# Kernel tuning notes

Measured on AMD Instinct MI355X. Metric: run time of the kernel, lower is better.

Reference implementation:

```python
import jax, jax.numpy as jnp
import numpy as np

S = 15.0  # hard-coded scale in HELoss.__init__


def setup_inputs() -> dict:
    key = jax.random.key(0)
    k1, k2, k3 = jax.random.split(key, 3)
    B, C = 4096, 32000
    logits = jax.random.normal(k1, (B, C), dtype=jnp.float32)
    labels = jax.random.randint(k2, (B,), 0, C, dtype=jnp.int64)
    cm = jax.random.uniform(k3, (), dtype=jnp.float32)
    return {"logits": logits, "labels": labels, "cm": cm}


def reference(logits, labels, cm):
    # logits: [B, C], labels: [B] int, cm: scalar margin
    B, C = logits.shape
    # diagonal gather: logits[i, labels[i]]
    tgt = jnp.take_along_axis(logits, labels[:, None], axis=1)[:, 0]  # [B]
    numerator = S * (tgt - cm)  # [B]
    # masked exp-sum over non-target classes (replaces the per-row cat loop)
    col = jnp.arange(C)[None, :]
    is_tgt = labels[:, None] == col  # [B, C] bool
    ex = jnp.where(is_tgt, 0.0, jnp.exp(S * logits))
    denom = jnp.exp(numerator) + jnp.sum(ex, axis=1)  # [B]
    return -jnp.mean(numerator - jnp.log(denom))
```

## Files before the change

### kernel.cpp

```cpp
#include <hip/hip_runtime.h>
#include <math.h>

#define SCALE_S 15.0f

__device__ __forceinline__ void combine_ms(float& m, float& s, float m2, float s2) {
    float nm = fmaxf(m, m2);
    s = s * __expf(m - nm) + s2 * __expf(m2 - nm);
    m = nm;
}

__global__ __launch_bounds__(256) void heloss_row_kernel(
        const float* __restrict__ logits,
        const int* __restrict__ labels,
        const float* __restrict__ cm_ptr,
        float* __restrict__ row_out,
        int C) {
    const int row = blockIdx.x;
    const int tid = threadIdx.x;
    const int label = labels[row];
    const float cm = cm_ptr[0];

    const long long row_base = (long long)row * (long long)C;
    const float4* rowp = reinterpret_cast<const float4*>(logits + row_base);
    const int nvec = C >> 2;

    float m = -INFINITY;
    float s = 0.0f;

    for (int f = tid; f < nvec; f += 256) {
        float4 v = rowp[f];
        int c0 = f << 2;
        float sv0 = (c0 + 0 == label) ? -INFINITY : SCALE_S * v.x;
        float sv1 = (c0 + 1 == label) ? -INFINITY : SCALE_S * v.y;
        float sv2 = (c0 + 2 == label) ? -INFINITY : SCALE_S * v.z;
        float sv3 = (c0 + 3 == label) ? -INFINITY : SCALE_S * v.w;
        float lm = fmaxf(fmaxf(sv0, sv1), fmaxf(sv2, sv3));
        float nm = fmaxf(m, lm);
        s = s * __expf(m - nm)
          + __expf(sv0 - nm) + __expf(sv1 - nm)
          + __expf(sv2 - nm) + __expf(sv3 - nm);
        m = nm;
    }

    #pragma unroll
    for (int off = 32; off >= 1; off >>= 1) {
        float m2 = __shfl_xor(m, off, 64);
        float s2 = __shfl_xor(s, off, 64);
        combine_ms(m, s, m2, s2);
    }

    __shared__ float sm[4], ss[4];
    const int wave = tid >> 6;
    const int lane = tid & 63;
    if (lane == 0) { sm[wave] = m; ss[wave] = s; }
    __syncthreads();

    if (tid == 0) {
        for (int w = 1; w < 4; ++w) combine_ms(m, s, sm[w], ss[w]);
        float tgt = logits[row_base + label];
        float num = SCALE_S * (tgt - cm);
        float tm = fmaxf(m, num);
        float denom = __expf(num - tm) + s * __expf(m - tm);
        float logdenom = tm + __logf(denom);
        row_out[row] = logdenom - num;
    }
}

__global__ __launch_bounds__(256) void heloss_mean_kernel(
        const float* __restrict__ rows, float* __restrict__ out, int B) {
    const int tid = threadIdx.x;
    float acc = 0.0f;
    for (int i = tid; i < B; i += 256) acc += rows[i];
    #pragma unroll
    for (int off = 32; off >= 1; off >>= 1) acc += __shfl_xor(acc, off, 64);
    __shared__ float w[4];
    if ((tid & 63) == 0) w[tid >> 6] = acc;
    __syncthreads();
    if (tid == 0) out[0] = (w[0] + w[1] + w[2] + w[3]) / (float)B;
}

extern "C" void kernel_launch(void* const* d_in, const int* in_sizes, int n_in,
                              void* d_out, int out_size, void* d_ws, size_t ws_size,
                              hipStream_t stream) {
    const float* logits = (const float*)d_in[0];
    const int* labels   = (const int*)d_in[1];
    const float* cm     = (const float*)d_in[2];
    float* out = (float*)d_out;
    float* ws  = (float*)d_ws;

    const int B = in_sizes[1];
    const int C = in_sizes[0] / B;

    heloss_row_kernel<<<dim3(B), dim3(256), 0, stream>>>(logits, labels, cm, ws, C);
    heloss_mean_kernel<<<dim3(1), dim3(256), 0, stream>>>(ws, out, B);
}
```

Baseline: 101.6 us.

## Replace online max-rescaled softmax with fixed-offset exp2 sum and nontemporal loads

```diff
diff --git a/kernel.cpp b/kernel.cpp
--- a/kernel.cpp
+++ b/kernel.cpp
@@ -1,13 +1,17 @@
 #include <hip/hip_runtime.h>
 #include <math.h>
 
-#define SCALE_S 15.0f
+typedef float f32x4 __attribute__((ext_vector_type(4)));
 
-__device__ __forceinline__ void combine_ms(float& m, float& s, float m2, float s2) {
-    float nm = fmaxf(m, m2);
-    s = s * __expf(m - nm) + s2 * __expf(m2 - nm);
-    m = nm;
-}
+#define S2F   21.640425613334451f
+#define KOFF  64.0f
+#define LN2F  0.6931471805599453f
+
+#if __has_builtin(__builtin_amdgcn_exp2f)
+#define EXP2(x) __builtin_amdgcn_exp2f(x)
+#else
+#define EXP2(x) exp2f(x)
+#endif
 
 __global__ __launch_bounds__(256) void heloss_row_kernel(
         const float* __restrict__ logits,
@@ -18,51 +22,40 @@
     const int row = blockIdx.x;
     const int tid = threadIdx.x;
     const int label = labels[row];
-    const float cm = cm_ptr[0];
-
     const long long row_base = (long long)row * (long long)C;
-    const float4* rowp = reinterpret_cast<const float4*>(logits + row_base);
+    const f32x4* rowp = reinterpret_cast<const f32x4*>(logits + row_base);
     const int nvec = C >> 2;
 
-    float m = -INFINITY;
-    float s = 0.0f;
+    float tgt = 0.0f;
+    if (tid == 0) tgt = logits[row_base + label];
 
+    float s0 = 0.f, s1 = 0.f, s2 = 0.f, s3 = 0.f;
     for (int f = tid; f < nvec; f += 256) {
-        float4 v = rowp[f];
+        f32x4 v = __builtin_nontemporal_load(rowp + f);
         int c0 = f << 2;
-        float sv0 = (c0 + 0 == label) ? -INFINITY : SCALE_S * v.x;
-        float sv1 = (c0 + 1 == label) ? -INFINITY : SCALE_S * v.y;
-        float sv2 = (c0 + 2 == label) ? -INFINITY : SCALE_S * v.z;
-        float sv3 = (c0 + 3 == label) ? -INFINITY : SCALE_S * v.w;
-        float lm = fmaxf(fmaxf(sv0, sv1), fmaxf(sv2, sv3));
-        float nm = fmaxf(m, lm);
-        s = s * __expf(m - nm)
-          + __expf(sv0 - nm) + __expf(sv1 - nm)
-          + __expf(sv2 - nm) + __expf(sv3 - nm);
-        m = nm;
+        float t0 = (c0 + 0 == label) ? -INFINITY : fmaf(S2F, v.x, -KOFF);
+        float t1 = (c0 + 1 == label) ? -INFINITY : fmaf(S2F, v.y, -KOFF);
+        float t2 = (c0 + 2 == label) ? -INFINITY : fmaf(S2F, v.z, -KOFF);
+        float t3 = (c0 + 3 == label) ? -INFINITY : fmaf(S2F, v.w, -KOFF);
+        s0 += EXP2(t0);
+        s1 += EXP2(t1);
+        s2 += EXP2(t2);
+        s3 += EXP2(t3);
     }
+    float s = (s0 + s1) + (s2 + s3);
 
     #pragma unroll
-    for (int off = 32; off >= 1; off >>= 1) {
-        float m2 = __shfl_xor(m, off, 64);
-        float s2 = __shfl_xor(s, off, 64);
-        combine_ms(m, s, m2, s2);
-    }
-
-    __shared__ float sm[4], ss[4];
-    const int wave = tid >> 6;
-    const int lane = tid & 63;
-    if (lane == 0) { sm[wave] = m; ss[wave] = s; }
+    for (int off = 32; off >= 1; off >>= 1) s += __shfl_xor(s, off, 64);
+    __shared__ float wsum[4];
+    if ((tid & 63) == 0) wsum[tid >> 6] = s;
     __syncthreads();
 
     if (tid == 0) {
-        for (int w = 1; w < 4; ++w) combine_ms(m, s, sm[w], ss[w]);
-        float tgt = logits[row_base + label];
-        float num = SCALE_S * (tgt - cm);
-        float tm = fmaxf(m, num);
-        float denom = __expf(num - tm) + s * __expf(m - tm);
-        float logdenom = tm + __logf(denom);
-        row_out[row] = logdenom - num;
+        float tot = (wsum[0] + wsum[1]) + (wsum[2] + wsum[3]);
+        float cm = cm_ptr[0];
+        float num2 = S2F * (tgt - cm);
+        float denom = tot + EXP2(num2 - KOFF);
+        row_out[row] = LN2F * (KOFF + log2f(denom) - num2);
     }
 }
 
```

Result: faster. 87.04 us (-14.4%).
